# Optimization experiments

Hardware: AMD Instinct MI355X
Metric: run time of the kernel (lower is better)

Reference implementation:

```python
import jax, jax.numpy as jnp
import numpy as np

G = 16          # graphs per side
NPG = 512       # nodes per graph
NSIDE = G * NPG # 8192 nodes per side
N = 2 * NSIDE   # 16384 nodes in combined batched graph
EPG = 4096      # edges per graph
E = 2 * G * EPG # 131072 edges
IN = 64; HID = 64; NH = 8; NC = 3
ALPHA = 0.2; EPS = 1e-5


def setup_inputs() -> dict:
    key = jax.random.key(0)
    ks = jax.random.split(key, 20)
    s = 0.05
    off = jnp.repeat(jnp.arange(2 * G, dtype=jnp.int32) * NPG, EPG)
    return {
        'nbd1': jax.random.normal(ks[0], (NSIDE, IN), jnp.float32),
        'nbd2': jax.random.normal(ks[1], (NSIDE, IN), jnp.float32),
        'ebd': jax.random.normal(ks[2], (E, IN), jnp.float32),
        'src': jax.random.randint(ks[3], (E,), 0, NPG, jnp.int32) + off,
        'dst': jax.random.randint(ks[4], (E,), 0, NPG, jnp.int32) + off,
        'node_gid': jnp.repeat(jnp.arange(2 * G, dtype=jnp.int32), NPG),
        'projW': jax.random.normal(ks[5], (4 * IN, HID), jnp.float32) * s,
        'W1': jax.random.normal(ks[6], (IN, NH * HID), jnp.float32) * s,
        'al1': jax.random.normal(ks[7], (NH, HID), jnp.float32) * s,
        'ar1': jax.random.normal(ks[8], (NH, HID), jnp.float32) * s,
        'ae1': jax.random.normal(ks[9], (NH, HID), jnp.float32) * s,
        'W2': jax.random.normal(ks[10], (NH * HID, NH * HID), jnp.float32) * s,
        'al2': jax.random.normal(ks[11], (NH, HID), jnp.float32) * s,
        'ar2': jax.random.normal(ks[12], (NH, HID), jnp.float32) * s,
        'ae2': jax.random.normal(ks[13], (NH, HID), jnp.float32) * s,
        'bn1_g': jnp.ones((2 * NH * HID,), jnp.float32),
        'bn1_b': jnp.zeros((2 * NH * HID,), jnp.float32),
        'fc1_W': jax.random.normal(ks[14], (2 * NH * HID, HID), jnp.float32) * s,
        'fc1_b': jnp.zeros((HID,), jnp.float32),
        'bn2_g': jnp.ones((HID,), jnp.float32),
        'bn2_b': jnp.zeros((HID,), jnp.float32),
        'fc2_W': jax.random.normal(ks[15], (HID, NC), jnp.float32) * s,
        'fc2_b': jnp.zeros((NC,), jnp.float32),
    }


def _segment_softmax(s, seg, n):
    # s: [E, H]; softmax over edges sharing the same destination node
    m = jax.ops.segment_max(s, seg, num_segments=n)
    ex = jnp.exp(s - m[seg])
    z = jax.ops.segment_sum(ex, seg, num_segments=n)
    return ex / jnp.maximum(z[seg], 1e-9)


def _gat_layer(hn, he, src, dst, n, W, al, ar, ae):
    nh, d = al.shape
    ft = (hn @ W).reshape(n, nh, d)            # [N,H,D]
    eft = (he @ W).reshape(-1, nh, d)          # [E,H,D]
    a1 = jnp.einsum('nhd,hd->nh', ft, al)
    a2 = jnp.einsum('nhd,hd->nh', ft, ar)
    a3 = jnp.einsum('ehd,hd->eh', eft, ae)
    a = a1[src] + a3 + a2[dst]                 # [E,H]
    a = jnp.where(a > 0, a, ALPHA * a)         # LeakyReLU(0.2)
    alpha = _segment_softmax(a, dst, n)[:, :, None]  # [E,H,1]
    f_cat = eft * alpha + ft[src] * alpha      # weighted edge + weighted src feat
    nft = jax.ops.segment_sum(f_cat, dst, num_segments=n)
    ret1 = jax.nn.elu(nft.reshape(n, nh * d))
    ret2 = jax.nn.elu(f_cat.reshape(f_cat.shape[0], nh * d))
    return ret1, ret2


def _bn(x, g, b):
    mu = jnp.mean(x, axis=0)
    v = jnp.var(x, axis=0)
    return (x - mu) * jax.lax.rsqrt(v + EPS) * g + b


def _forward(nbd1, nbd2, ebd, src, dst, node_gid, projW,
             W1, al1, ar1, ae1, W2, al2, ar2, ae2,
             bn1_g, bn1_b, fc1_W, fc1_b, bn2_g, bn2_b, fc2_W, fc2_b):
    # Node alignment (cross-graph soft attention, 2-D tensors as in source)
    att = nbd1 @ nbd2.T                                   # [N1,N2]
    x1a = jax.nn.softmax(att, axis=-1) @ nbd2
    x2a = jax.nn.softmax(att.T, axis=-1) @ nbd1
    q1 = jnp.concatenate([nbd1, x1a, nbd1 - x1a, nbd1 * x1a], axis=-1)
    q2 = jnp.concatenate([nbd2, x2a, nbd2 - x2a, nbd2 * x2a], axis=-1)
    h1 = jax.nn.relu(q1 @ projW)
    h2 = jax.nn.relu(q2 @ projW)
    h_n = jnp.concatenate([h1, h2], axis=0)               # [N,HID]
    h_e = ebd
    h_n, h_e = _gat_layer(h_n, h_e, src, dst, N, W1, al1, ar1, ae1)
    h_n, h_e = _gat_layer(h_n, h_e, src, dst, N, W2, al2, ar2, ae2)
    # dgl.mean_nodes
    cnt = jax.ops.segment_sum(jnp.ones((N,), h_n.dtype), node_gid, num_segments=2 * G)
    hg = jax.ops.segment_sum(h_n, node_gid, num_segments=2 * G) / cnt[:, None]
    x = jnp.concatenate([hg[:G], hg[G:2 * G]], axis=1)    # [G, 2*NH*HID]
    x = _bn(x, bn1_g, bn1_b)
    x = jax.nn.relu(x @ fc1_W + fc1_b)
    x = _bn(x, bn2_g, bn2_b)
    return x @ fc2_W + fc2_b                              # [G, NC]


def reference(nbd1, nbd2, ebd, src, dst, node_gid, projW,
              W1, al1, ar1, ae1, W2, al2, ar2, ae2,
              bn1_g, bn1_b, fc1_W, fc1_b, bn2_g, bn2_b, fc2_W, fc2_b):
    return _forward(nbd1, nbd2, ebd, src, dst, node_gid, projW,
                    W1, al1, ar1, ae1, W2, al2, ar2, ae2,
                    bn1_g, bn1_b, fc1_W, fc1_b, bn2_g, bn2_b, fc2_W, fc2_b)
```

## Files before the change

kernel.cpp:

```cpp
#include <hip/hip_runtime.h>


#define NSd 8192
#define NNd 16384
#define NEd 131072
#define KSPLIT 8

typedef unsigned short u16;
typedef unsigned int   u32;
typedef short bf16x8 __attribute__((ext_vector_type(8)));
typedef float f32x4  __attribute__((ext_vector_type(4)));
typedef float f32x16 __attribute__((ext_vector_type(16)));

__device__ __forceinline__ float bf2f(u16 u){ return __uint_as_float(((u32)u) << 16); }
__device__ __forceinline__ u16 f2bf(float f){
  u32 u = __float_as_uint(f);
  u += 0x7fffu + ((u >> 16) & 1u);
  return (u16)(u >> 16);
}
__device__ __forceinline__ u32 pkbf(float a, float b){
  u32 r;
  asm("v_cvt_pk_bf16_f32 %0, %1, %2" : "=v"(r) : "v"(a), "v"(b));
  return r;
}
__device__ __forceinline__ void pl32swap(u32& a, u32& b){
  auto r = __builtin_amdgcn_permlane32_swap(a, b, false, false);
  a = r[0]; b = r[1];
}
__device__ __forceinline__ float eluf(float x){ return x > 0.f ? x : expm1f(x); }
__device__ __forceinline__ float leaky(float x){ return x > 0.f ? x : 0.2f * x; }
__device__ __forceinline__ float ldin(const void* p, size_t i, int fl){
  return fl ? bf2f(((const u16*)p)[i]) : ((const float*)p)[i];
}
__device__ __forceinline__ void lse_merge(float& m, float& z, float om, float oz){
  float M = fmaxf(m, om);
  z = z * __expf(m - M) + oz * __expf(om - M);
  m = M;
}

static constexpr size_t OFF_WF   = 0;
static constexpr size_t OFF_CB   = 1529600;
static constexpr size_t OFF_U    = 1584896;
static constexpr size_t OFF_W1B  = 18362112;
static constexpr size_t OFF_W2B  = 18427648;
static constexpr size_t OFF_WE2B = 18951936;
static constexpr size_t OFF_WE1B = 18968320;
static constexpr size_t OFF_AL1  = 35139328;
static constexpr size_t OFF_SA   = 39333632;
static constexpr size_t OFF_HNA  = 43527936;
static constexpr size_t OFF_DEG  = 77082368;
static constexpr size_t OFF_RP   = 77147904;
static constexpr size_t OFF_FILL = 77213696;
static constexpr size_t OFF_CIDX = 77279232;
static constexpr size_t OFF_RBIG = 77803520;
static constexpr size_t OFF_T    = 111357952;
static constexpr size_t OFF_XCAT = 144912384;
static constexpr size_t OFF_FLAG = 144977920;
static constexpr size_t WS_NEED  = 144978176;

static constexpr size_t T_X1A = 0;
static constexpr size_t T_X2A = 2097152;
static constexpr size_t T_HN0 = 4194304;
static constexpr size_t T_PZ  = 4194304;
static constexpr size_t T_AN1 = 8388608;
static constexpr size_t T_S   = 9437184;
static constexpr size_t T_Y   = 0;
static constexpr size_t T_Y1G = 0;
static constexpr size_t R_AN2 = 17301504;
static constexpr size_t R_G2  = 18350080;

static constexpr int WO_PROJ = 0,      WO_W1 = 16384;
static constexpr int WO_AL1 = 49152,   WO_AR1 = 49664,  WO_AE1 = 50176;
static constexpr int WO_W2  = 50688;
static constexpr int WO_AL2 = 312832,  WO_AR2 = 313344, WO_AE2 = 313856;
static constexpr int WO_B1G = 314368,  WO_B1B = 315392;
static constexpr int WO_F1W = 316416,  WO_F1B = 381952;
static constexpr int WO_B2G = 382016,  WO_B2B = 382080;
static constexpr int WO_F2W = 382144,  WO_F2B = 382336;
static constexpr int WO_END = 382339;

static constexpr int CB_WC1 = 0;
static constexpr int CB_WE1 = 1024;
static constexpr int CB_WC2 = 1536;
static constexpr int CB_WE2 = 9728;
static constexpr int CB_END = 13824;

__global__ __launch_bounds__(256) void detect_k(const u16* __restrict__ p, int* __restrict__ flag){
  __shared__ int bad;
  if (threadIdx.x == 0) bad = 0;
  __syncthreads();
  int b = 0;
  for (int i = threadIdx.x; i < 1024; i += 256){
    float f = bf2f(p[i]);
    if (!(fabsf(f) <= 100.f)) b++;
  }
  atomicAdd(&bad, b);
  __syncthreads();
  if (threadIdx.x == 0) *flag = (bad == 0) ? 1 : 0;
}

struct P17 { const void* p[17]; };

__global__ __launch_bounds__(256) void convw_k(P17 ps, float* __restrict__ wf, const int* __restrict__ flagp){
  const int i = blockIdx.x * 256 + threadIdx.x;
  if (i >= WO_END) return;
  const int fl = *flagp;
  const int ends[17] = {16384,49152,49664,50176,50688,312832,313344,313856,314368,
                        315392,316416,381952,382016,382080,382144,382336,382339};
  int seg = 0;
  while (i >= ends[seg]) seg++;
  const int start = seg ? ends[seg-1] : 0;
  wf[i] = ldin(ps.p[seg], i - start, fl);
}

__global__ __launch_bounds__(256) void convwT_k(const float* __restrict__ wf, u16* __restrict__ w1t,
                                                u16* __restrict__ w2t){
  const int i = blockIdx.x * 256 + threadIdx.x;
  if (i < 32768){
    const int c = i >> 6, k = i & 63;
    w1t[i] = f2bf(wf[WO_W1 + k * 512 + c]);
  } else if (i < 32768 + 262144){
    const int j = i - 32768;
    const int c = j >> 9, k = j & 511;
    w2t[j] = f2bf(wf[WO_W2 + k * 512 + c]);
  }
}

__global__ __launch_bounds__(256) void combos_k(const float* __restrict__ wf, float* __restrict__ cb,
                                                u16* __restrict__ we2b, u16* __restrict__ we1b){
  const int i = blockIdx.x * 256 + threadIdx.x;
  if (i >= CB_END + 4096 + 512) return;
  if (i >= CB_END + 4096){ we1b[512 + (i - CB_END - 4096)] = 0; return; }
  if (i >= CB_END){ we2b[4096 + (i - CB_END)] = 0; return; }
  float acc = 0.f;
  if (i < 1024){
    const int o = i >> 6, d = i & 63, h = o & 7;
    const float* a = wf + ((o >> 3) ? WO_AR1 : WO_AL1) + h * 64;
    for (int dp = 0; dp < 64; dp++) acc += wf[WO_W1 + d * 512 + h * 64 + dp] * a[dp];
    cb[CB_WC1 + i] = acc;
  } else if (i < 1536){
    const int j = i - 1024, h = j >> 6, d = j & 63;
    for (int dp = 0; dp < 64; dp++) acc += wf[WO_W1 + d * 512 + h * 64 + dp] * wf[WO_AE1 + h * 64 + dp];
    cb[CB_WE1 + j] = acc;
    we1b[j] = f2bf(acc);
  } else if (i < 9728){
    const int j = i - 1536, o = j >> 9, c = j & 511, h = o & 7;
    for (int dp = 0; dp < 64; dp++){
      const float av = (o >> 3) ? wf[WO_AR2 + h * 64 + dp]
                                : (wf[WO_AL2 + h * 64 + dp] - wf[WO_AE2 + h * 64 + dp]);
      acc += wf[WO_W2 + c * 512 + h * 64 + dp] * av;
    }
    cb[CB_WC2 + j] = acc;
  } else {
    const int j = i - 9728, h = j >> 9, c = j & 511;
    for (int dp = 0; dp < 64; dp++) acc += wf[WO_W2 + c * 512 + h * 64 + dp] * wf[WO_AE2 + h * 64 + dp];
    cb[CB_WE2 + j] = acc;
    we2b[j] = f2bf(acc);
  }
}

__global__ __launch_bounds__(256) void flash_mfma_k(const void* __restrict__ Qp, const void* __restrict__ Kp,
                                                    const int* __restrict__ flagp, float* __restrict__ pacc,
                                                    float* __restrict__ pz){
  const int fl = *flagp;
  __shared__ __align__(16) u16 Ks[2][32][64];
  __shared__ __align__(16) u16 Kt[2][64][40];
  const int t = threadIdx.x;
  const int w = t >> 6, l = t & 63;
  const int hi = l >> 5, ql = l & 31;
  const int q0 = blockIdx.x * 128;
  const int kbeg = blockIdx.y * 1024;
  const int sr = t & 31, scg = t >> 5;
  const int kp = t & 15, dq = t >> 4;

  bf16x8 bq[4];
  {
    const int qrow = q0 + w * 32 + ql;
    if (fl){
      const u16* qp = (const u16*)Qp + (size_t)qrow * 64 + hi * 8;
      #pragma unroll
      for (int s = 0; s < 4; s++) bq[s] = *(const bf16x8*)(qp + s * 16);
    } else {
      const float* qp = (const float*)Qp + (size_t)qrow * 64 + hi * 8;
      #pragma unroll
      for (int s = 0; s < 4; s++){
        union { u32 w_[4]; bf16x8 v; } u;
        #pragma unroll
        for (int i = 0; i < 4; i++) u.w_[i] = pkbf(qp[s*16 + 2*i], qp[s*16 + 2*i + 1]);
        bq[s] = u.v;
      }
    }
  }

  f32x16 accO0, accO1;
  #pragma unroll
  for (int i = 0; i < 16; i++){ accO0[i] = 0.f; accO1[i] = 0.f; }
  float lsum = 0.f;

  {
    const int kr = kbeg;
    if (fl){
      const u16* kb = (const u16*)Kp + (size_t)kr * 64;
      const uint4 s0 = *(const uint4*)(kb + (size_t)sr * 64 + scg * 8);
      const uint2 a0 = *(const uint2*)(kb + (size_t)(2*kp) * 64 + dq * 4);
      const uint2 b0 = *(const uint2*)(kb + (size_t)(2*kp + 1) * 64 + dq * 4);
      *(uint4*)((char*)&Ks[0][sr][0] + ((scg * 16) ^ ((sr & 7) << 4))) = s0;
      const u16* pa = (const u16*)&a0; const u16* pb = (const u16*)&b0;
      #pragma unroll
      for (int i = 0; i < 4; i++)
        *(u32*)&Kt[0][4*dq + i][2*kp] = (u32)pa[i] | ((u32)pb[i] << 16);
    } else {
      const float* kf = (const float*)Kp + (size_t)kr * 64;
      const float4 f0 = *(const float4*)(kf + (size_t)sr * 64 + scg * 8);
      const float4 f1 = *(const float4*)(kf + (size_t)sr * 64 + scg * 8 + 4);
      const float4 fa = *(const float4*)(kf + (size_t)(2*kp) * 64 + dq * 4);
      const float4 fb = *(const float4*)(kf + (size_t)(2*kp + 1) * 64 + dq * 4);
      union { u32 w_[4]; uint4 q; } uu;
      uu.w_[0] = pkbf(f0.x, f0.y); uu.w_[1] = pkbf(f0.z, f0.w);
      uu.w_[2] = pkbf(f1.x, f1.y); uu.w_[3] = pkbf(f1.z, f1.w);
      *(uint4*)((char*)&Ks[0][sr][0] + ((scg * 16) ^ ((sr & 7) << 4))) = uu.q;
      const float* faf = &fa.x; const float* fbf = &fb.x;
      #pragma unroll
      for (int i = 0; i < 4; i++)
        *(u32*)&Kt[0][4*dq + i][2*kp] = pkbf(faf[i], fbf[i]);
    }
  }

  for (int it = 0; it < 32; it++){
    const int cur = it & 1;
    __syncthreads();

    uint4 nKs; uint2 nKa, nKb;
    float4 nKsf0, nKsf1, nKaf, nKbf;
    const bool nx = (it + 1 < 32);
    if (nx){
      const int kr = kbeg + (it + 1) * 32;
      if (fl){
        const u16* kb = (const u16*)Kp + (size_t)kr * 64;
        nKs = *(const uint4*)(kb + (size_t)sr * 64 + scg * 8);
        nKa = *(const uint2*)(kb + (size_t)(2*kp) * 64 + dq * 4);
        nKb = *(const uint2*)(kb + (size_t)(2*kp + 1) * 64 + dq * 4);
      } else {
        const float* kf = (const float*)Kp + (size_t)kr * 64;
        nKsf0 = *(const float4*)(kf + (size_t)sr * 64 + scg * 8);
        nKsf1 = *(const float4*)(kf + (size_t)sr * 64 + scg * 8 + 4);
        nKaf  = *(const float4*)(kf + (size_t)(2*kp) * 64 + dq * 4);
        nKbf  = *(const float4*)(kf + (size_t)(2*kp + 1) * 64 + dq * 4);
      }
    }

    f32x16 accS;
    #pragma unroll
    for (int i = 0; i < 16; i++) accS[i] = 0.f;
    #pragma unroll
    for (int s = 0; s < 4; s++){
      const int byo = (s * 32 + hi * 16) ^ ((ql & 7) << 4);
      const bf16x8 a = *(const bf16x8*)((const char*)&Ks[cur][ql][0] + byo);
      accS = __builtin_amdgcn_mfma_f32_32x32x16_bf16(a, bq[s], accS, 0, 0, 0);
    }
    float p[16];
    #pragma unroll
    for (int r = 0; r < 16; r++) p[r] = exp2f(fmaf(accS[r], 1.44269504f, -46.1662413f));
    {
      const float s0 = (p[0] + p[1]) + (p[2] + p[3]);
      const float s1 = (p[4] + p[5]) + (p[6] + p[7]);
      const float s2 = (p[8] + p[9]) + (p[10] + p[11]);
      const float s3 = (p[12] + p[13]) + (p[14] + p[15]);
      lsum += (s0 + s1) + (s2 + s3);
    }
    u32 pk_[8];
    #pragma unroll
    for (int j = 0; j < 4; j++){
      pk_[2*j]     = pkbf(p[4*j],     p[4*j + 1]);
      pk_[2*j + 1] = pkbf(p[4*j + 2], p[4*j + 3]);
    }
    pl32swap(pk_[0], pk_[2]); pl32swap(pk_[1], pk_[3]);
    pl32swap(pk_[4], pk_[6]); pl32swap(pk_[5], pk_[7]);
    union { u32 w_[4]; bf16x8 v; } ua, ub;
    ua.w_[0] = pk_[0]; ua.w_[1] = pk_[1]; ua.w_[2] = pk_[2]; ua.w_[3] = pk_[3];
    ub.w_[0] = pk_[4]; ub.w_[1] = pk_[5]; ub.w_[2] = pk_[6]; ub.w_[3] = pk_[7];
    {
      const u16* kt0 = &Kt[cur][ql][hi * 8];
      accO0 = __builtin_amdgcn_mfma_f32_32x32x16_bf16(ua.v, *(const bf16x8*)kt0, accO0, 0, 0, 0);
      accO0 = __builtin_amdgcn_mfma_f32_32x32x16_bf16(ub.v, *(const bf16x8*)(kt0 + 16), accO0, 0, 0, 0);
      const u16* kt1 = &Kt[cur][32 + ql][hi * 8];
      accO1 = __builtin_amdgcn_mfma_f32_32x32x16_bf16(ua.v, *(const bf16x8*)kt1, accO1, 0, 0, 0);
      accO1 = __builtin_amdgcn_mfma_f32_32x32x16_bf16(ub.v, *(const bf16x8*)(kt1 + 16), accO1, 0, 0, 0);
    }

    if (nx){
      char* kd = (char*)&Ks[cur ^ 1][sr][0];
      const int byo = (scg * 16) ^ ((sr & 7) << 4);
      if (fl){
        *(uint4*)(kd + byo) = nKs;
        const u16* pa = (const u16*)&nKa; const u16* pb = (const u16*)&nKb;
        #pragma unroll
        for (int i = 0; i < 4; i++)
          *(u32*)&Kt[cur ^ 1][4*dq + i][2*kp] = (u32)pa[i] | ((u32)pb[i] << 16);
      } else {
        union { u32 w_[4]; uint4 q; } uu;
        uu.w_[0] = pkbf(nKsf0.x, nKsf0.y); uu.w_[1] = pkbf(nKsf0.z, nKsf0.w);
        uu.w_[2] = pkbf(nKsf1.x, nKsf1.y); uu.w_[3] = pkbf(nKsf1.z, nKsf1.w);
        *(uint4*)(kd + byo) = uu.q;
        const float* faf = &nKaf.x; const float* fbf = &nKbf.x;
        #pragma unroll
        for (int i = 0; i < 4; i++)
          *(u32*)&Kt[cur ^ 1][4*dq + i][2*kp] = pkbf(faf[i], fbf[i]);
      }
    }
  }

  const float zq = lsum + __shfl_xor(lsum, 32);
  const int rowb = q0 + w * 32;
  #pragma unroll
  for (int r = 0; r < 16; r++){
    const int m = (r & 3) + 8 * (r >> 2) + 4 * hi;
    float* pr = pacc + ((size_t)blockIdx.y * NSd + rowb + m) * 64;
    pr[ql]      = accO0[r];
    pr[32 + ql] = accO1[r];
  }
  if (hi == 0) pz[blockIdx.y * NSd + rowb + ql] = zq;
}

__global__ __launch_bounds__(256) void flash_merge_k(const float* __restrict__ pacc,
                                                     const float* __restrict__ pz, float* __restrict__ outp){
  const int t = threadIdx.x;
  const int r = blockIdx.x * 4 + (t >> 6);
  const int d = t & 63;
  float Zt = 0.f, v = 0.f;
  #pragma unroll
  for (int s = 0; s < KSPLIT; s++){
    Zt += pz[s * NSd + r];
    v  += pacc[((size_t)s * NSd + r) * 64 + d];
  }
  outp[(size_t)r * 64 + d] = v / Zt;
}

__global__ __launch_bounds__(256) void proj_k(const void* __restrict__ nbd1, const void* __restrict__ nbd2,
                                              const float* __restrict__ x1a, const float* __restrict__ x2a,
                                              const float* __restrict__ wf, float* __restrict__ hn0,
                                              const int* __restrict__ flagp){
  const int fl = *flagp;
  __shared__ float At[64][65], Bt[64][65];
  const int t = threadIdx.x, tx = t & 15, ty = t >> 4;
  const int m0 = blockIdx.x * 64;
  float acc[4][4] = {{0.f}};
  for (int kt = 0; kt < 256; kt += 64){
    __syncthreads();
    {
      const int i = t >> 2, c0 = (t & 3) * 16;
      const int mrow = m0 + i;
      const int side = mrow < NSd;
      const int mr = side ? mrow : mrow - NSd;
      const void* nb = side ? nbd1 : nbd2;
      const float* xa = side ? x1a : x2a;
      const int seg = kt >> 6;
      for (int c = 0; c < 16; c++){
        const int kk = c0 + c;
        const float nv = ldin(nb, (size_t)mr * 64 + kk, fl);
        const float av = xa[(size_t)mr * 64 + kk];
        At[i][kk] = (seg == 0) ? nv : (seg == 1) ? av : (seg == 2) ? (nv - av) : (nv * av);
      }
      const int kk = t >> 2;
      for (int c = 0; c < 16; c++) Bt[kk][c0 + c] = wf[WO_PROJ + (kt + kk) * 64 + c0 + c];
    }
    __syncthreads();
    #pragma unroll
    for (int k = 0; k < 64; k++){
      float a0 = At[ty*4+0][k], a1 = At[ty*4+1][k], a2 = At[ty*4+2][k], a3 = At[ty*4+3][k];
      float b0 = Bt[k][tx*4+0], b1 = Bt[k][tx*4+1], b2 = Bt[k][tx*4+2], b3 = Bt[k][tx*4+3];
      acc[0][0] = fmaf(a0,b0,acc[0][0]); acc[0][1] = fmaf(a0,b1,acc[0][1]); acc[0][2] = fmaf(a0,b2,acc[0][2]); acc[0][3] = fmaf(a0,b3,acc[0][3]);
      acc[1][0] = fmaf(a1,b0,acc[1][0]); acc[1][1] = fmaf(a1,b1,acc[1][1]); acc[1][2] = fmaf(a1,b2,acc[1][2]); acc[1][3] = fmaf(a1,b3,acc[1][3]);
      acc[2][0] = fmaf(a2,b0,acc[2][0]); acc[2][1] = fmaf(a2,b1,acc[2][1]); acc[2][2] = fmaf(a2,b2,acc[2][2]); acc[2][3] = fmaf(a2,b3,acc[2][3]);
      acc[3][0] = fmaf(a3,b0,acc[3][0]); acc[3][1] = fmaf(a3,b1,acc[3][1]); acc[3][2] = fmaf(a3,b2,acc[3][2]); acc[3][3] = fmaf(a3,b3,acc[3][3]);
    }
  }
  #pragma unroll
  for (int i = 0; i < 4; i++)
    #pragma unroll
    for (int j = 0; j < 4; j++)
      hn0[(size_t)(m0 + ty*4 + i) * 64 + tx*4 + j] = fmaxf(acc[i][j], 0.f);
}

__global__ __launch_bounds__(256) void an64_k(const float* __restrict__ hn0, const float* __restrict__ wc,
                                              float* __restrict__ an){
  const int id = blockIdx.x * 256 + threadIdx.x;
  const int n = id >> 4, o = id & 15;
  const float* row = hn0 + (size_t)n * 64;
  const float* wp = wc + o * 64;
  float acc = 0.f;
  for (int k = 0; k < 64; k += 4){
    const float4 r4 = *(const float4*)(row + k);
    const float4 w4 = *(const float4*)(wp + k);
    acc += r4.x*w4.x + r4.y*w4.y + r4.z*w4.z + r4.w*w4.w;
  }
  an[id] = acc;
}

__global__ __launch_bounds__(256) void anw_k(const float* __restrict__ HNA, const float* __restrict__ wc,
                                             float* __restrict__ an){
  __shared__ float W[16][516];
  const int t = threadIdx.x;
  for (int i = t; i < 8192; i += 256) W[i >> 9][i & 511] = wc[i];
  __syncthreads();
  const int node = blockIdx.x * 64 + (t >> 2);
  const int cb0 = (t & 3) * 4;
  const float* row = HNA + (size_t)node * 512;
  float acc[4] = {0.f, 0.f, 0.f, 0.f};
  for (int k = 0; k < 512; k += 4){
    const float4 r = *(const float4*)(row + k);
    #pragma unroll
    for (int j = 0; j < 4; j++){
      const float* wr = &W[cb0 + j][k];
      acc[j] += r.x * wr[0] + r.y * wr[1] + r.z * wr[2] + r.w * wr[3];
    }
  }
  #pragma unroll
  for (int j = 0; j < 4; j++) an[node * 16 + cb0 + j] = acc[j];
}

__global__ __launch_bounds__(256) void us1_k(const void* __restrict__ ebd, const float* __restrict__ hn0,
                                             const int* __restrict__ src, u16* __restrict__ Ub,
                                             const int* __restrict__ flagp){
  const int fl = *flagp;
  const int id = blockIdx.x * 256 + threadIdx.x;
  const int e = id >> 4, q = id & 15, d0 = q * 4;
  const int sn = src[e];
  float ev[4];
  if (fl){
    const uint2 u = *(const uint2*)((const u16*)ebd + (size_t)e * 64 + d0);
    ev[0] = bf2f((u16)(u.x & 0xffffu)); ev[1] = bf2f((u16)(u.x >> 16));
    ev[2] = bf2f((u16)(u.y & 0xffffu)); ev[3] = bf2f((u16)(u.y >> 16));
  } else {
    const float4 f = *(const float4*)((const float*)ebd + (size_t)e * 64 + d0);
    ev[0] = f.x; ev[1] = f.y; ev[2] = f.z; ev[3] = f.w;
  }
  const float4 hv = *(const float4*)(hn0 + (size_t)sn * 64 + d0);
  ushort4 o;
  o.x = f2bf(ev[0] + hv.x); o.y = f2bf(ev[1] + hv.y);
  o.z = f2bf(ev[2] + hv.z); o.w = f2bf(ev[3] + hv.w);
  *(ushort4*)(Ub + (size_t)e * 64 + d0) = o;
}

__global__ __launch_bounds__(256) void score1_k(const void* __restrict__ ebd, const u16* __restrict__ we1b,
                                                const float* __restrict__ an, const int* __restrict__ src,
                                                const int* __restrict__ dst, const int* __restrict__ cidx,
                                                float* __restrict__ S, const int* __restrict__ flagp){
  __shared__ int Se[64], De[64], Ee[64];
  const int t = threadIdx.x;
  const int w = t >> 6, lane = t & 63;
  const int col = lane & 15, quad = lane >> 4;
  const int p0 = blockIdx.x * 64;
  if (t < 64){ const int e = cidx[p0 + t]; Ee[t] = e; Se[t] = src[e]; De[t] = dst[e]; }
  __syncthreads();
  const int fl = *flagp;
  const int ea = Ee[w*16 + col];
  bf16x8 a0, a1;
  if (fl){
    const u16* ap = (const u16*)ebd + (size_t)ea * 64;
    a0 = *(const bf16x8*)(ap + quad*8);
    a1 = *(const bf16x8*)(ap + 32 + quad*8);
  } else {
    const float* ap = (const float*)ebd + (size_t)ea * 64;
    union { u32 w_[4]; bf16x8 v; } u0, u1;
    #pragma unroll
    for (int i = 0; i < 4; i++){
      u0.w_[i] = pkbf(ap[quad*8 + 2*i],      ap[quad*8 + 2*i + 1]);
      u1.w_[i] = pkbf(ap[32 + quad*8 + 2*i], ap[32 + quad*8 + 2*i + 1]);
    }
    a0 = u0.v; a1 = u1.v;
  }
  const u16* brow = we1b + (size_t)col * 64;
  const bf16x8 b0 = *(const bf16x8*)(brow + quad*8);
  const bf16x8 b1 = *(const bf16x8*)(brow + 32 + quad*8);
  f32x4 acc = (f32x4){0.f, 0.f, 0.f, 0.f};
  acc = __builtin_amdgcn_mfma_f32_16x16x32_bf16(a0, b0, acc, 0, 0, 0);
  acc = __builtin_amdgcn_mfma_f32_16x16x32_bf16(a1, b1, acc, 0, 0, 0);
  if (col < 8){
    #pragma unroll
    for (int i = 0; i < 4; i++){
      const int rl = w*16 + quad*4 + i;
      S[(size_t)(p0 + rl) * 8 + col] = leaky(an[Se[rl]*16 + col] + acc[i] + an[De[rl]*16 + 8 + col]);
    }
  }
}

__global__ __launch_bounds__(256) void segalpha_pos_k(const float* __restrict__ S, const int* __restrict__ rp,
                                                      float* __restrict__ AL){
  const int node = blockIdx.x * 4 + (threadIdx.x >> 6);
  const int l = threadIdx.x & 63;
  const int h = l & 7, i0 = l >> 3;
  const int beg = rp[node], end = rp[node + 1];
  float m = -1e30f, z = 0.f;
  for (int base = beg; base < end; base += 8){
    const int idx = base + i0;
    float v = -1e30f, cc = 0.f;
    if (idx < end){ v = S[(size_t)idx * 8 + h]; cc = 1.f; }
    lse_merge(m, z, v, cc);
  }
  #pragma unroll
  for (int off = 8; off < 64; off <<= 1){
    float om = __shfl_xor(m, off), oz = __shfl_xor(z, off);
    lse_merge(m, z, om, oz);
  }
  const float rz = 1.f / fmaxf(z, 1e-9f);
  for (int base = beg; base < end; base += 8){
    const int idx = base + i0;
    if (idx < end)
      AL[(size_t)idx * 8 + h] = __expf(S[(size_t)idx * 8 + h] - m) * rz;
  }
}

__global__ __launch_bounds__(256) void g1b_k(const float* __restrict__ AL, const u16* __restrict__ Ub,
                                             const int* __restrict__ rp, const int* __restrict__ cidx,
                                             u16* __restrict__ G1b){
  const int n = blockIdx.x;
  const int t = threadIdx.x;
  const int d = t & 63, hh = t >> 6;
  const int beg = rp[n], end = rp[n + 1];
  float a0 = 0.f, a1 = 0.f;
  for (int idx = beg; idx < end; idx++){
    const int e = cidx[idx];
    const float uv = bf2f(Ub[(size_t)e * 64 + d]);
    a0 = fmaf(AL[(size_t)idx * 8 + hh],     uv, a0);
    a1 = fmaf(AL[(size_t)idx * 8 + hh + 4], uv, a1);
  }
  G1b[(size_t)(n * 8 + hh)     * 64 + d] = f2bf(a0);
  G1b[(size_t)(n * 8 + hh + 4) * 64 + d] = f2bf(a1);
}

__global__ __launch_bounds__(256) void nft1m_k(const u16* __restrict__ G1b, const u16* __restrict__ W1T,
                                               float* __restrict__ HNA){
  const int t = threadIdx.x;
  const int w = t >> 6, lane = t & 63;
  const int col = lane & 15, quad = lane >> 4;
  const int h = blockIdx.y;
  const int nl0 = blockIdx.x * 32;
  const int mt = (w & 1) * 16;
  const int nb = (w >> 1) * 2;
  const u16* arow = G1b + ((size_t)(nl0 + mt + col) * 8 + h) * 64;
  const bf16x8 a0 = *(const bf16x8*)(arow + quad*8);
  const bf16x8 a1 = *(const bf16x8*)(arow + 32 + quad*8);
  #pragma unroll
  for (int nn = 0; nn < 2; nn++){
    const int nt = nb + nn;
    const u16* brow = W1T + (size_t)(h*64 + nt*16 + col) * 64;
    const bf16x8 b0 = *(const bf16x8*)(brow + quad*8);
    const bf16x8 b1 = *(const bf16x8*)(brow + 32 + quad*8);
    f32x4 acc = (f32x4){0.f, 0.f, 0.f, 0.f};
    acc = __builtin_amdgcn_mfma_f32_16x16x32_bf16(a0, b0, acc, 0, 0, 0);
    acc = __builtin_amdgcn_mfma_f32_16x16x32_bf16(a1, b1, acc, 0, 0, 0);
    #pragma unroll
    for (int i = 0; i < 4; i++)
      HNA[(size_t)(nl0 + mt + quad*4 + i) * 512 + h*64 + nt*16 + col] = eluf(acc[i]);
  }
}

__global__ __launch_bounds__(256) void y3_k(const u16* __restrict__ Ub, const float* __restrict__ AL1,
                                            const float* __restrict__ HNA, const u16* __restrict__ W1T,
                                            const int* __restrict__ src, const int* __restrict__ cidx,
                                            u16* __restrict__ Y, const int s2){
  __shared__ __align__(16) u16 Us[32][72];
  __shared__ float als[256];
  __shared__ int Es[32], Ss[32];
  const int t = threadIdx.x;
  const int w = t >> 6, lane = t & 63;
  const int col = lane & 15, quad = lane >> 4;
  const int mw = (w & 1) * 16;
  const int hw = (w >> 1) * 4;
  const int ep0 = s2 * 32768 + blockIdx.x * 32;
  if (t < 32){ const int e = cidx[ep0 + t]; Es[t] = e; Ss[t] = src[e]; }
  als[t] = AL1[(size_t)ep0 * 8 + t];
  __syncthreads();
  {
    const int r = t >> 3, seg = (t & 7) * 8;
    *(ushort4*)&Us[r][seg]     = *(const ushort4*)(Ub + (size_t)Es[r] * 64 + seg);
    *(ushort4*)&Us[r][seg + 4] = *(const ushort4*)(Ub + (size_t)Es[r] * 64 + seg + 4);
  }
  __syncthreads();
  const bf16x8 a0 = *(const bf16x8*)&Us[mw + col][quad*8];
  const bf16x8 a1 = *(const bf16x8*)&Us[mw + col][32 + quad*8];
  #pragma unroll
  for (int hh = 0; hh < 4; hh++){
    const int h = hw + hh;
    #pragma unroll
    for (int nt = 0; nt < 4; nt++){
      const u16* brow = W1T + (size_t)(h*64 + nt*16 + col) * 64;
      const bf16x8 b0 = *(const bf16x8*)(brow + quad*8);
      const bf16x8 b1 = *(const bf16x8*)(brow + 32 + quad*8);
      f32x4 acc = (f32x4){0.f, 0.f, 0.f, 0.f};
      acc = __builtin_amdgcn_mfma_f32_16x16x32_bf16(a0, b0, acc, 0, 0, 0);
      acc = __builtin_amdgcn_mfma_f32_16x16x32_bf16(a1, b1, acc, 0, 0, 0);
      #pragma unroll
      for (int i = 0; i < 4; i++){
        const int er = mw + quad*4 + i;
        const float v = eluf(als[er*8 + h] * acc[i]) + HNA[(size_t)Ss[er] * 512 + h*64 + nt*16 + col];
        Y[(size_t)(blockIdx.x*32 + er) * 512 + h*64 + nt*16 + col] = f2bf(v);
      }
    }
  }
}

__global__ __launch_bounds__(256) void score2_k(const u16* __restrict__ Y, const u16* __restrict__ we2b,
                                                const float* __restrict__ AN2, const int* __restrict__ src,
                                                const int* __restrict__ dst, const int* __restrict__ cidx,
                                                float* __restrict__ SA, const int s2){
  __shared__ int Se[64], De[64];
  const int t = threadIdx.x;
  const int w = t >> 6, lane = t & 63;
  const int col = lane & 15, quad = lane >> 4;
  const int p0 = blockIdx.x * 64;
  const int gbase = s2 * 32768;
  if (t < 64){ const int e = cidx[gbase + p0 + t]; Se[t] = src[e]; De[t] = dst[e]; }
  __syncthreads();
  const u16* arow = Y + (size_t)(p0 + w*16 + col) * 512;
  const u16* brow = we2b + (size_t)col * 512;
  f32x4 acc = (f32x4){0.f, 0.f, 0.f, 0.f};
  #pragma unroll
  for (int ks = 0; ks < 16; ks++){
    const bf16x8 a = *(const bf16x8*)(arow + ks*32 + quad*8);
    const bf16x8 b = *(const bf16x8*)(brow + ks*32 + quad*8);
    acc = __builtin_amdgcn_mfma_f32_16x16x32_bf16(a, b, acc, 0, 0, 0);
  }
  if (col < 8){
    #pragma unroll
    for (int i = 0; i < 4; i++){
      const int rl = w*16 + quad*4 + i;
      const size_t pos = gbase + p0 + rl;
      SA[pos * 8 + col] = leaky(AN2[Se[rl]*16 + col] + acc[i] + AN2[De[rl]*16 + 8 + col]);
    }
  }
}

__global__ __launch_bounds__(256) void sg2_k(const u16* __restrict__ Y, const int* __restrict__ rp,
                                             const float* __restrict__ SA, u16* __restrict__ G2,
                                             const int s){
  __shared__ float sc[64][8];
  __shared__ float mh[8], rzh[8];
  const int t = threadIdx.x;
  const int nl = blockIdx.x;
  const int n = s * 2048 + nl;
  const int beg = rp[n], end = rp[n + 1], m = end - beg;
  const int base = (s >> 1) * 32768;
  const bool small = (m <= 64);
  {
    const int h = t >> 5, l32 = t & 31;
    float mm = -1e30f, zz = 0.f;
    for (int i = l32; i < m; i += 32)
      lse_merge(mm, zz, SA[(size_t)(beg + i) * 8 + h], 1.f);
    #pragma unroll
    for (int off = 1; off < 32; off <<= 1){
      const float om = __shfl_xor(mm, off), oz = __shfl_xor(zz, off);
      lse_merge(mm, zz, om, oz);
    }
    if (l32 == 0){ mh[h] = mm; rzh[h] = 1.f / fmaxf(zz, 1e-9f); }
  }
  __syncthreads();
  if (small){
    for (int idx = t; idx < m * 8; idx += 256){
      const int i = idx >> 3, h = idx & 7;
      sc[i][h] = __expf(SA[(size_t)(beg + i) * 8 + h] - mh[h]) * rzh[h];
    }
  }
  __syncthreads();
  {
    const int d0 = t * 2;
    float ac[8][2] = {{0.f}};
    for (int i = 0; i < m; i++){
      const int epl = beg + i - base;
      const u32 yv = *(const u32*)(Y + (size_t)epl * 512 + d0);
      const float y0 = bf2f((u16)(yv & 0xffffu)), y1 = bf2f((u16)(yv >> 16));
      float al[8];
      if (small){
        #pragma unroll
        for (int h = 0; h < 8; h++) al[h] = sc[i][h];
      } else {
        #pragma unroll
        for (int h = 0; h < 8; h++)
          al[h] = __expf(SA[(size_t)(beg + i) * 8 + h] - mh[h]) * rzh[h];
      }
      #pragma unroll
      for (int h = 0; h < 8; h++){
        ac[h][0] = fmaf(al[h], y0, ac[h][0]);
        ac[h][1] = fmaf(al[h], y1, ac[h][1]);
      }
    }
    #pragma unroll
    for (int h = 0; h < 8; h++){
      const u32 o = (u32)f2bf(ac[h][0]) | ((u32)f2bf(ac[h][1]) << 16);
      *(u32*)(G2 + ((size_t)nl * 8 + h) * 512 + d0) = o;
    }
  }
}

__global__ __launch_bounds__(256) void nft2m_k(const u16* __restrict__ G2, const u16* __restrict__ W2T,
                                               u16* __restrict__ HNB, const int s){
  const int t = threadIdx.x;
  const int w = t >> 6, lane = t & 63;
  const int col = lane & 15, quad = lane >> 4;
  const int h = blockIdx.y;
  const int nl0 = blockIdx.x * 32;
  const int mt = (w & 1) * 16;
  const int nb = (w >> 1) * 2;
  const u16* arow = G2 + ((size_t)((nl0 + mt + col) * 8) + h) * 512;
  #pragma unroll
  for (int nn = 0; nn < 2; nn++){
    const int nt = nb + nn;
    const u16* brow = W2T + (size_t)(h*64 + nt*16 + col) * 512;
    f32x4 acc = (f32x4){0.f, 0.f, 0.f, 0.f};
    #pragma unroll
    for (int ks = 0; ks < 16; ks++){
      const bf16x8 a = *(const bf16x8*)(arow + ks*32 + quad*8);
      const bf16x8 b = *(const bf16x8*)(brow + ks*32 + quad*8);
      acc = __builtin_amdgcn_mfma_f32_16x16x32_bf16(a, b, acc, 0, 0, 0);
    }
    #pragma unroll
    for (int i = 0; i < 4; i++)
      HNB[(size_t)(s*2048 + nl0 + mt + quad*4 + i) * 512 + h*64 + nt*16 + col] = f2bf(eluf(acc[i]));
  }
}

__global__ __launch_bounds__(256) void hist_k(const int* __restrict__ dst, int* __restrict__ deg){
  const int e = blockIdx.x * 256 + threadIdx.x;
  if (e < NEd) atomicAdd(&deg[dst[e]], 1);
}
__global__ __launch_bounds__(256) void scan_k(const int* __restrict__ deg, int* __restrict__ rp,
                                              int* __restrict__ fill){
  __shared__ int wsum[4];
  const int t = threadIdx.x;
  const int lane = t & 63, wid = t >> 6;
  const int base = t * 64;
  int s = 0;
  for (int i = 0; i < 64; i++) s += deg[base + i];
  int v = s;
  #pragma unroll
  for (int off = 1; off < 64; off <<= 1){
    const int u = __shfl_up(v, off);
    if (lane >= off) v += u;
  }
  if (lane == 63) wsum[wid] = v;
  __syncthreads();
  int add = 0;
  #pragma unroll
  for (int wq = 0; wq < 4; wq++) if (wq < wid) add += wsum[wq];
  int off0 = add + v - s;
  for (int i = 0; i < 64; i++){
    rp[base + i] = off0; fill[base + i] = off0;
    off0 += deg[base + i];
  }
  if (t == 255) rp[NNd] = off0;
}
__global__ __launch_bounds__(256) void scatter_k(const int* __restrict__ dst, int* __restrict__ fill,
                                                 int* __restrict__ cidx){
  const int e = blockIdx.x * 256 + threadIdx.x;
  if (e < NEd){
    int pos = atomicAdd(&fill[dst[e]], 1);
    cidx[pos] = e;
  }
}

__global__ __launch_bounds__(256) void mean_k(const u16* __restrict__ HNB, float* __restrict__ xcat){
  const int sg = blockIdx.x >> 3, chunk = blockIdx.x & 7;
  const int t = threadIdx.x;
  const int g = (sg < 16) ? sg : sg - 16;
  const int half = (sg < 16) ? 0 : 1;
  const int c0 = t * 2;
  float s0 = 0.f, s1 = 0.f;
  const u16* base = HNB + ((size_t)sg * 512 + chunk * 64) * 512;
  for (int n = 0; n < 64; n++){
    const u32 u = *(const u32*)(base + (size_t)n * 512 + c0);
    s0 += bf2f((u16)(u & 0xffffu));
    s1 += bf2f((u16)(u >> 16));
  }
  atomicAdd(&xcat[g * 1024 + half * 512 + c0],     s0 * (1.f / 512.f));
  atomicAdd(&xcat[g * 1024 + half * 512 + c0 + 1], s1 * (1.f / 512.f));
}

__global__ __launch_bounds__(256) void bn1_k(float* __restrict__ xcat, const float* __restrict__ wf){
  const int j = blockIdx.x * 256 + threadIdx.x;
  float mu = 0.f;
  #pragma unroll
  for (int g = 0; g < 16; g++) mu += xcat[g * 1024 + j];
  mu *= (1.f / 16.f);
  float var = 0.f;
  #pragma unroll
  for (int g = 0; g < 16; g++){ const float d = xcat[g * 1024 + j] - mu; var += d * d; }
  var *= (1.f / 16.f);
  const float sc = rsqrtf(var + 1e-5f) * wf[WO_B1G + j];
  const float sh = wf[WO_B1B + j] - mu * sc;
  #pragma unroll
  for (int g = 0; g < 16; g++) xcat[g * 1024 + j] = xcat[g * 1024 + j] * sc + sh;
}

__global__ __launch_bounds__(256) void fc1_k(const float* __restrict__ xcat, const float* __restrict__ wf,
                                             float* __restrict__ y1g){
  __shared__ float xs[1024];
  __shared__ float ps[4][64];
  const int t = threadIdx.x, g = blockIdx.x;
  for (int i = t; i < 1024; i += 256) xs[i] = xcat[g * 1024 + i];
  __syncthreads();
  const int c = t & 63, kq = t >> 6;
  float acc = 0.f;
  #pragma unroll 4
  for (int k = kq * 256; k < kq * 256 + 256; k++)
    acc = fmaf(xs[k], wf[WO_F1W + k * 64 + c], acc);
  ps[kq][c] = acc;
  __syncthreads();
  if (t < 64){
    const float a = ps[0][t] + ps[1][t] + ps[2][t] + ps[3][t] + wf[WO_F1B + t];
    y1g[g * 64 + t] = fmaxf(a, 0.f);
  }
}

__global__ __launch_bounds__(256) void head2_k(const float* __restrict__ y1g, const float* __restrict__ wf,
                                               void* __restrict__ outp, const int* __restrict__ flagp){
  __shared__ float y1s[16][64];
  __shared__ float mu2s[64], sc2s[64];
  const int t = threadIdx.x;
  for (int i = t; i < 1024; i += 256) y1s[i >> 6][i & 63] = y1g[i];
  __syncthreads();
  if (t < 64){
    float mu = 0.f;
    #pragma unroll
    for (int g = 0; g < 16; g++) mu += y1s[g][t];
    mu *= (1.f / 16.f);
    float var = 0.f;
    #pragma unroll
    for (int g = 0; g < 16; g++){ const float d = y1s[g][t] - mu; var += d * d; }
    var *= (1.f / 16.f);
    mu2s[t] = mu; sc2s[t] = rsqrtf(var + 1e-5f) * wf[WO_B2G + t];
  }
  __syncthreads();
  if (t < 48){
    const int gg = t / 3, c = t % 3;
    float acc = wf[WO_F2B + c];
    #pragma unroll
    for (int k = 0; k < 64; k++){
      const float y2 = (y1s[gg][k] - mu2s[k]) * sc2s[k] + wf[WO_B2B + k];
      acc = fmaf(y2, wf[WO_F2W + k * 3 + c], acc);
    }
    if (*flagp) ((u16*)outp)[t] = f2bf(acc);
    else        ((float*)outp)[t] = acc;
  }
}

extern "C" void kernel_launch(void* const* d_in, const int* in_sizes, int n_in,
                              void* d_out, int out_size, void* d_ws, size_t ws_size,
                              hipStream_t stream) {
  (void)in_sizes; (void)n_in; (void)out_size;
  if (ws_size < WS_NEED) return;

  const int* src = (const int*)d_in[3];
  const int* dst = (const int*)d_in[4];
  char* w = (char*)d_ws;

  float* wf   = (float*)(w + OFF_WF);
  float* cb   = (float*)(w + OFF_CB);
  u16*   Ub   = (u16*)(w + OFF_U);
  u16*   W1T  = (u16*)(w + OFF_W1B);
  u16*   W2T  = (u16*)(w + OFF_W2B);
  u16*   we2b = (u16*)(w + OFF_WE2B);
  u16*   we1b = (u16*)(w + OFF_WE1B);
  float* AL1  = (float*)(w + OFF_AL1);
  float* SA   = (float*)(w + OFF_SA);
  float* HNA  = (float*)(w + OFF_HNA);
  int*   deg  = (int*)(w + OFF_DEG);
  int*   rp   = (int*)(w + OFF_RP);
  int*   fill = (int*)(w + OFF_FILL);
  int*   cidx = (int*)(w + OFF_CIDX);
  float* rbig = (float*)(w + OFF_RBIG);
  float* xcat = (float*)(w + OFF_XCAT);
  int*   flag = (int*)(w + OFF_FLAG);

  float* x1a  = (float*)(w + OFF_T + T_X1A);
  float* x2a  = (float*)(w + OFF_T + T_X2A);
  float* hn0  = (float*)(w + OFF_T + T_HN0);
  float* AN1  = (float*)(w + OFF_T + T_AN1);
  float* S    = (float*)(w + OFF_T + T_S);
  u16*   Y    = (u16*)(w + OFF_T + T_Y);
  float* y1g  = (float*)(w + OFF_T + T_Y1G);

  float* pacc = rbig;
  float* pz   = (float*)(w + OFF_T + T_PZ);
  u16*   G1b  = (u16*)(w + OFF_RBIG);
  u16*   HNB  = (u16*)(w + OFF_RBIG);
  float* AN2  = (float*)(w + OFF_RBIG + R_AN2);
  u16*   G2   = (u16*)(w + OFF_RBIG + R_G2);

  detect_k<<<1, 256, 0, stream>>>((const u16*)d_in[0], flag);
  P17 ps;
  for (int i = 0; i < 17; i++) ps.p[i] = d_in[6 + i];
  convw_k<<<(WO_END + 255) / 256, 256, 0, stream>>>(ps, wf, flag);
  convwT_k<<<(32768 + 262144 + 255) / 256, 256, 0, stream>>>(wf, W1T, W2T);
  combos_k<<<(CB_END + 4096 + 512 + 255) / 256, 256, 0, stream>>>(wf, cb, we2b, we1b);

  hipMemsetAsync(deg, 0, NNd * sizeof(int), stream);
  hist_k<<<NEd / 256, 256, 0, stream>>>(dst, deg);
  scan_k<<<1, 256, 0, stream>>>(deg, rp, fill);
  scatter_k<<<NEd / 256, 256, 0, stream>>>(dst, fill, cidx);

  flash_mfma_k<<<dim3(64, KSPLIT), 256, 0, stream>>>(d_in[0], d_in[1], flag, pacc, pz);
  flash_merge_k<<<NSd / 4, 256, 0, stream>>>(pacc, pz, x1a);
  flash_mfma_k<<<dim3(64, KSPLIT), 256, 0, stream>>>(d_in[1], d_in[0], flag, pacc, pz);
  flash_merge_k<<<NSd / 4, 256, 0, stream>>>(pacc, pz, x2a);

  proj_k<<<NNd / 64, 256, 0, stream>>>(d_in[0], d_in[1], x1a, x2a, wf, hn0, flag);

  an64_k<<<NNd * 16 / 256, 256, 0, stream>>>(hn0, cb + CB_WC1, AN1);
  us1_k<<<NEd * 16 / 256, 256, 0, stream>>>(d_in[2], hn0, src, Ub, flag);
  score1_k<<<NEd / 64, 256, 0, stream>>>(d_in[2], we1b, AN1, src, dst, cidx, S, flag);
  segalpha_pos_k<<<NNd / 4, 256, 0, stream>>>(S, rp, AL1);
  g1b_k<<<NNd, 256, 0, stream>>>(AL1, Ub, rp, cidx, G1b);
  nft1m_k<<<dim3(NNd / 32, 8), 256, 0, stream>>>(G1b, W1T, HNA);

  anw_k<<<NNd / 64, 256, 0, stream>>>(HNA, cb + CB_WC2, AN2);

  for (int s2 = 0; s2 < 4; s2++){
    y3_k<<<1024, 256, 0, stream>>>(Ub, AL1, HNA, W1T, src, cidx, Y, s2);
    score2_k<<<512, 256, 0, stream>>>(Y, we2b, AN2, src, dst, cidx, SA, s2);
    for (int sub = 0; sub < 2; sub++){
      const int s = s2 * 2 + sub;
      sg2_k<<<2048, 256, 0, stream>>>(Y, rp, SA, G2, s);
      nft2m_k<<<dim3(64, 8), 256, 0, stream>>>(G2, W2T, HNB, s);
    }
  }

  hipMemsetAsync(xcat, 0, 16 * 1024 * sizeof(float), stream);
  mean_k<<<256, 256, 0, stream>>>(HNB, xcat);
  bn1_k<<<4, 256, 0, stream>>>(xcat, wf);
  fc1_k<<<16, 256, 0, stream>>>(xcat, wf, y1g);
  head2_k<<<1, 256, 0, stream>>>(y1g, wf, d_out, flag);
}
```

Baseline: 819.9 us.

## Store layer-1 node features as bf16 and fuse small prep/BN kernels

```diff
diff --git a/kernel.cpp b/kernel.cpp
--- a/kernel.cpp
+++ b/kernel.cpp
@@ -48,6 +48,7 @@
 static constexpr size_t OFF_AL1  = 35139328;
 static constexpr size_t OFF_SA   = 39333632;
 static constexpr size_t OFF_HNA  = 43527936;
+static constexpr size_t OFF_AN2  = 60305152;
 static constexpr size_t OFF_DEG  = 77082368;
 static constexpr size_t OFF_RP   = 77147904;
 static constexpr size_t OFF_FILL = 77213696;
@@ -66,8 +67,7 @@
 static constexpr size_t T_S   = 9437184;
 static constexpr size_t T_Y   = 0;
 static constexpr size_t T_Y1G = 0;
-static constexpr size_t R_AN2 = 17301504;
-static constexpr size_t R_G2  = 18350080;
+static constexpr size_t R_G2  = 16777216;
 
 static constexpr int WO_PROJ = 0,      WO_W1 = 16384;
 static constexpr int WO_AL1 = 49152,   WO_AR1 = 49664,  WO_AE1 = 50176;
@@ -113,49 +113,49 @@
   wf[i] = ldin(ps.p[seg], i - start, fl);
 }
 
-__global__ __launch_bounds__(256) void convwT_k(const float* __restrict__ wf, u16* __restrict__ w1t,
-                                                u16* __restrict__ w2t){
+__global__ __launch_bounds__(256) void wprep_k(const float* __restrict__ wf, u16* __restrict__ w1t,
+                                               u16* __restrict__ w2t, float* __restrict__ cb,
+                                               u16* __restrict__ we2b, u16* __restrict__ we1b){
   const int i = blockIdx.x * 256 + threadIdx.x;
   if (i < 32768){
     const int c = i >> 6, k = i & 63;
     w1t[i] = f2bf(wf[WO_W1 + k * 512 + c]);
-  } else if (i < 32768 + 262144){
+    return;
+  }
+  if (i < 294912){
     const int j = i - 32768;
     const int c = j >> 9, k = j & 511;
     w2t[j] = f2bf(wf[WO_W2 + k * 512 + c]);
-  }
-}
-
-__global__ __launch_bounds__(256) void combos_k(const float* __restrict__ wf, float* __restrict__ cb,
-                                                u16* __restrict__ we2b, u16* __restrict__ we1b){
-  const int i = blockIdx.x * 256 + threadIdx.x;
-  if (i >= CB_END + 4096 + 512) return;
-  if (i >= CB_END + 4096){ we1b[512 + (i - CB_END - 4096)] = 0; return; }
-  if (i >= CB_END){ we2b[4096 + (i - CB_END)] = 0; return; }
+    return;
+  }
+  const int j = i - 294912;
+  if (j >= CB_END + 4096 + 512) return;
+  if (j >= CB_END + 4096){ we1b[512 + (j - CB_END - 4096)] = 0; return; }
+  if (j >= CB_END){ we2b[4096 + (j - CB_END)] = 0; return; }
   float acc = 0.f;
-  if (i < 1024){
-    const int o = i >> 6, d = i & 63, h = o & 7;
+  if (j < 1024){
+    const int o = j >> 6, d = j & 63, h = o & 7;
     const float* a = wf + ((o >> 3) ? WO_AR1 : WO_AL1) + h * 64;
     for (int dp = 0; dp < 64; dp++) acc += wf[WO_W1 + d * 512 + h * 64 + dp] * a[dp];
-    cb[CB_WC1 + i] = acc;
-  } else if (i < 1536){
-    const int j = i - 1024, h = j >> 6, d = j & 63;
+    cb[CB_WC1 + j] = acc;
+  } else if (j < 1536){
+    const int jj = j - 1024, h = jj >> 6, d = jj & 63;
     for (int dp = 0; dp < 64; dp++) acc += wf[WO_W1 + d * 512 + h * 64 + dp] * wf[WO_AE1 + h * 64 + dp];
-    cb[CB_WE1 + j] = acc;
-    we1b[j] = f2bf(acc);
-  } else if (i < 9728){
-    const int j = i - 1536, o = j >> 9, c = j & 511, h = o & 7;
+    cb[CB_WE1 + jj] = acc;
+    we1b[jj] = f2bf(acc);
+  } else if (j < 9728){
+    const int jj = j - 1536, o = jj >> 9, c = jj & 511, h = o & 7;
     for (int dp = 0; dp < 64; dp++){
       const float av = (o >> 3) ? wf[WO_AR2 + h * 64 + dp]
                                 : (wf[WO_AL2 + h * 64 + dp] - wf[WO_AE2 + h * 64 + dp]);
       acc += wf[WO_W2 + c * 512 + h * 64 + dp] * av;
     }
-    cb[CB_WC2 + j] = acc;
+    cb[CB_WC2 + jj] = acc;
   } else {
-    const int j = i - 9728, h = j >> 9, c = j & 511;
+    const int jj = j - 9728, h = jj >> 9, c = jj & 511;
     for (int dp = 0; dp < 64; dp++) acc += wf[WO_W2 + c * 512 + h * 64 + dp] * wf[WO_AE2 + h * 64 + dp];
-    cb[CB_WE2 + j] = acc;
-    we2b[j] = f2bf(acc);
+    cb[CB_WE2 + jj] = acc;
+    we2b[jj] = f2bf(acc);
   }
 }
 
@@ -397,7 +397,7 @@
   an[id] = acc;
 }
 
-__global__ __launch_bounds__(256) void anw_k(const float* __restrict__ HNA, const float* __restrict__ wc,
+__global__ __launch_bounds__(256) void anw_k(const u16* __restrict__ HNA, const float* __restrict__ wc,
                                              float* __restrict__ an){
   __shared__ float W[16][516];
   const int t = threadIdx.x;
@@ -405,14 +405,16 @@
   __syncthreads();
   const int node = blockIdx.x * 64 + (t >> 2);
   const int cb0 = (t & 3) * 4;
-  const float* row = HNA + (size_t)node * 512;
+  const u16* row = HNA + (size_t)node * 512;
   float acc[4] = {0.f, 0.f, 0.f, 0.f};
   for (int k = 0; k < 512; k += 4){
-    const float4 r = *(const float4*)(row + k);
+    const uint2 u = *(const uint2*)(row + k);
+    const float r0 = bf2f((u16)(u.x & 0xffffu)), r1 = bf2f((u16)(u.x >> 16));
+    const float r2 = bf2f((u16)(u.y & 0xffffu)), r3 = bf2f((u16)(u.y >> 16));
     #pragma unroll
     for (int j = 0; j < 4; j++){
       const float* wr = &W[cb0 + j][k];
-      acc[j] += r.x * wr[0] + r.y * wr[1] + r.z * wr[2] + r.w * wr[3];
+      acc[j] += r0 * wr[0] + r1 * wr[1] + r2 * wr[2] + r3 * wr[3];
     }
   }
   #pragma unroll
@@ -530,7 +532,7 @@
 }
 
 __global__ __launch_bounds__(256) void nft1m_k(const u16* __restrict__ G1b, const u16* __restrict__ W1T,
-                                               float* __restrict__ HNA){
+                                               u16* __restrict__ HNA){
   const int t = threadIdx.x;
   const int w = t >> 6, lane = t & 63;
   const int col = lane & 15, quad = lane >> 4;
@@ -552,12 +554,12 @@
     acc = __builtin_amdgcn_mfma_f32_16x16x32_bf16(a1, b1, acc, 0, 0, 0);
     #pragma unroll
     for (int i = 0; i < 4; i++)
-      HNA[(size_t)(nl0 + mt + quad*4 + i) * 512 + h*64 + nt*16 + col] = eluf(acc[i]);
+      HNA[(size_t)(nl0 + mt + quad*4 + i) * 512 + h*64 + nt*16 + col] = f2bf(eluf(acc[i]));
   }
 }
 
 __global__ __launch_bounds__(256) void y3_k(const u16* __restrict__ Ub, const float* __restrict__ AL1,
-                                            const float* __restrict__ HNA, const u16* __restrict__ W1T,
+                                            const u16* __restrict__ HNA, const u16* __restrict__ W1T,
                                             const int* __restrict__ src, const int* __restrict__ cidx,
                                             u16* __restrict__ Y, const int s2){
   __shared__ __align__(16) u16 Us[32][72];
@@ -594,7 +596,8 @@
       #pragma unroll
       for (int i = 0; i < 4; i++){
         const int er = mw + quad*4 + i;
-        const float v = eluf(als[er*8 + h] * acc[i]) + HNA[(size_t)Ss[er] * 512 + h*64 + nt*16 + col];
+        const float v = eluf(als[er*8 + h] * acc[i])
+                      + bf2f(HNA[(size_t)Ss[er] * 512 + h*64 + nt*16 + col]);
         Y[(size_t)(blockIdx.x*32 + er) * 512 + h*64 + nt*16 + col] = f2bf(v);
       }
     }
@@ -776,28 +779,23 @@
   atomicAdd(&xcat[g * 1024 + half * 512 + c0 + 1], s1 * (1.f / 512.f));
 }
 
-__global__ __launch_bounds__(256) void bn1_k(float* __restrict__ xcat, const float* __restrict__ wf){
-  const int j = blockIdx.x * 256 + threadIdx.x;
-  float mu = 0.f;
-  #pragma unroll
-  for (int g = 0; g < 16; g++) mu += xcat[g * 1024 + j];
-  mu *= (1.f / 16.f);
-  float var = 0.f;
-  #pragma unroll
-  for (int g = 0; g < 16; g++){ const float d = xcat[g * 1024 + j] - mu; var += d * d; }
-  var *= (1.f / 16.f);
-  const float sc = rsqrtf(var + 1e-5f) * wf[WO_B1G + j];
-  const float sh = wf[WO_B1B + j] - mu * sc;
-  #pragma unroll
-  for (int g = 0; g < 16; g++) xcat[g * 1024 + j] = xcat[g * 1024 + j] * sc + sh;
-}
-
 __global__ __launch_bounds__(256) void fc1_k(const float* __restrict__ xcat, const float* __restrict__ wf,
                                              float* __restrict__ y1g){
   __shared__ float xs[1024];
   __shared__ float ps[4][64];
   const int t = threadIdx.x, g = blockIdx.x;
-  for (int i = t; i < 1024; i += 256) xs[i] = xcat[g * 1024 + i];
+  for (int j = t; j < 1024; j += 256){
+    float mu = 0.f;
+    #pragma unroll
+    for (int gg = 0; gg < 16; gg++) mu += xcat[gg * 1024 + j];
+    mu *= (1.f / 16.f);
+    float var = 0.f;
+    #pragma unroll
+    for (int gg = 0; gg < 16; gg++){ const float d = xcat[gg * 1024 + j] - mu; var += d * d; }
+    var *= (1.f / 16.f);
+    const float sc = rsqrtf(var + 1e-5f) * wf[WO_B1G + j];
+    xs[j] = (xcat[g * 1024 + j] - mu) * sc + wf[WO_B1B + j];
+  }
   __syncthreads();
   const int c = t & 63, kq = t >> 6;
   float acc = 0.f;
@@ -863,7 +861,8 @@
   u16*   we1b = (u16*)(w + OFF_WE1B);
   float* AL1  = (float*)(w + OFF_AL1);
   float* SA   = (float*)(w + OFF_SA);
-  float* HNA  = (float*)(w + OFF_HNA);
+  u16*   HNA  = (u16*)(w + OFF_HNA);
+  float* AN2  = (float*)(w + OFF_AN2);
   int*   deg  = (int*)(w + OFF_DEG);
   int*   rp   = (int*)(w + OFF_RP);
   int*   fill = (int*)(w + OFF_FILL);
@@ -884,15 +883,13 @@
   float* pz   = (float*)(w + OFF_T + T_PZ);
   u16*   G1b  = (u16*)(w + OFF_RBIG);
   u16*   HNB  = (u16*)(w + OFF_RBIG);
-  float* AN2  = (float*)(w + OFF_RBIG + R_AN2);
   u16*   G2   = (u16*)(w + OFF_RBIG + R_G2);
 
   detect_k<<<1, 256, 0, stream>>>((const u16*)d_in[0], flag);
   P17 ps;
   for (int i = 0; i < 17; i++) ps.p[i] = d_in[6 + i];
   convw_k<<<(WO_END + 255) / 256, 256, 0, stream>>>(ps, wf, flag);
-  convwT_k<<<(32768 + 262144 + 255) / 256, 256, 0, stream>>>(wf, W1T, W2T);
-  combos_k<<<(CB_END + 4096 + 512 + 255) / 256, 256, 0, stream>>>(wf, cb, we2b, we1b);
+  wprep_k<<<(294912 + CB_END + 4096 + 512 + 255) / 256, 256, 0, stream>>>(wf, W1T, W2T, cb, we2b, we1b);
 
   hipMemsetAsync(deg, 0, NNd * sizeof(int), stream);
   hist_k<<<NEd / 256, 256, 0, stream>>>(dst, deg);
@@ -927,7 +924,6 @@
 
   hipMemsetAsync(xcat, 0, 16 * 1024 * sizeof(float), stream);
   mean_k<<<256, 256, 0, stream>>>(HNB, xcat);
-  bn1_k<<<4, 256, 0, stream>>>(xcat, wf);
   fc1_k<<<16, 256, 0, stream>>>(xcat, wf, y1g);
   head2_k<<<1, 256, 0, stream>>>(y1g, wf, d_out, flag);
 }
```

Result: no change. 810.5 us (-1.1%).
